# Optimization experiments

Measured on AMD Instinct MI355X. Metric: run time of the kernel, lower is better.

Reference implementation:

```python
import jax, jax.numpy as jnp
import numpy as np

D_LOW = 32
LAGS = [1, 2, 4, 8]
# Upper-triangular pair indices (offset=1), matching torch.triu_indices(d_low, d_low, 1)
IDX_I, IDX_J = np.triu_indices(D_LOW, k=1)
IDX_I = jnp.asarray(IDX_I)
IDX_J = jnp.asarray(IDX_J)
EPS = 1e-6


def setup_inputs() -> dict:
    key = jax.random.key(0)
    ks = jax.random.split(key, 7)
    b, n, d_model = 4, 4096, 1024
    d_plucker = D_LOW * (D_LOW - 1) // 2  # 496
    s = lambda fan_in: 1.0 / np.sqrt(fan_in)
    return {
        "x": jax.random.normal(ks[0], (b, n, d_model), dtype=jnp.float32),
        "W_red": jax.random.normal(ks[1], (d_model, D_LOW), dtype=jnp.float32) * s(d_model),
        "b_red": jax.random.normal(ks[2], (D_LOW,), dtype=jnp.float32) * s(d_model),
        "W_exp": jax.random.normal(ks[3], (d_plucker, d_model), dtype=jnp.float32) * s(d_plucker),
        "b_exp": jax.random.normal(ks[4], (d_model,), dtype=jnp.float32) * s(d_plucker),
        "W_gate": jax.random.normal(ks[5], (2 * d_model, d_model), dtype=jnp.float32) * s(2 * d_model),
        "b_gate": jax.random.normal(ks[6], (d_model,), dtype=jnp.float32) * s(2 * d_model),
    }


def reference(x, W_red, b_red, W_exp, b_exp, W_gate, b_gate):
    b, n, _ = x.shape
    d_plucker = D_LOW * (D_LOW - 1) // 2
    z = x @ W_red + b_red  # [b, n, d_low]
    plucker_total = jnp.zeros((b, n, d_plucker), dtype=x.dtype)
    counts = jnp.zeros((b, n, 1), dtype=x.dtype)
    for lag in LAGS:
        if lag <= 0 or lag >= n:
            continue
        z_curr = z[:, lag:, :]   # [b, n-lag, d_low]
        z_past = z[:, :-lag, :]  # [b, n-lag, d_low]
        # Antisymmetric Plucker coordinates over upper-triangular index pairs
        p = (z_curr[:, :, IDX_I] * z_past[:, :, IDX_J]
             - z_curr[:, :, IDX_J] * z_past[:, :, IDX_I])  # [b, n-lag, d_plucker]
        norm = jnp.linalg.norm(p, axis=-1, keepdims=True)
        p = p / jnp.maximum(norm, EPS)
        plucker_total = plucker_total.at[:, lag:, :].add(p)
        counts = counts.at[:, lag:, :].add(1.0)
    counts = jnp.maximum(counts, 1.0)
    plucker_avg = plucker_total / counts
    g_avg = plucker_avg @ W_exp + b_exp  # [b, n, d_model]
    concat = jnp.concatenate([x, g_avg], axis=-1)  # [b, n, 2*d_model]
    gate = jax.nn.sigmoid(concat @ W_gate + b_gate)
    return gate * x + (1.0 - gate) * g_avg
```

## Files before the change

kernel.cpp:

```cpp
#include <hip/hip_runtime.h>
#include <hip/hip_bf16.h>
#include <math.h>

#define B_DIM   4
#define N_DIM   4096
#define D_MODEL 1024
#define D_LOW   32
#define NPAIR   496
#define NROWS   (B_DIM * N_DIM)
#define KPAD3   512
#define LDA2    1536

typedef __bf16 bf16;
typedef __bf16 bf16x8 __attribute__((ext_vector_type(8)));
typedef __bf16 bf16x4 __attribute__((ext_vector_type(4)));
typedef float  f32x4  __attribute__((ext_vector_type(4)));

#define GLOAD_LDS16(g, l) __builtin_amdgcn_global_load_lds( \
    (__attribute__((address_space(1))) void*)(g),           \
    (__attribute__((address_space(3))) void*)(l), 16, 0, 0)

__global__ __launch_bounds__(256) void prep_misc(const float* __restrict__ Wr,
                                                 bf16* __restrict__ WrT,
                                                 const float* __restrict__ We,
                                                 const float* __restrict__ be,
                                                 bf16* __restrict__ WeB) {
    __shared__ float tile[32][33];
    const int bx = blockIdx.x;
    const int t  = threadIdx.x;
    if (bx < 32) {
        const int kb = bx * 32;
        {
            int k = t >> 3, c4 = (t & 7) * 4;
            float4 v = *reinterpret_cast<const float4*>(&Wr[(size_t)(kb + k) * 32 + c4]);
            tile[k][c4 + 0] = v.x; tile[k][c4 + 1] = v.y;
            tile[k][c4 + 2] = v.z; tile[k][c4 + 3] = v.w;
        }
        __syncthreads();
        {
            int c = t >> 3, kq = (t & 7) * 4;
            bf16x4 o = { (bf16)tile[kq + 0][c], (bf16)tile[kq + 1][c],
                         (bf16)tile[kq + 2][c], (bf16)tile[kq + 3][c] };
            *reinterpret_cast<bf16x4*>(&WrT[(size_t)c * 1024 + kb + kq]) = o;
        }
    } else {
        size_t o = ((size_t)(bx - 32) * 256 + t) * 4;
        int row = (int)(o >> 10), col = (int)(o & 1023);
        float4 v = {0.f, 0.f, 0.f, 0.f};
        if (row < NPAIR)       v = *reinterpret_cast<const float4*>(&We[(size_t)row * 1024 + col]);
        else if (row == NPAIR) v = *reinterpret_cast<const float4*>(&be[col]);
        bf16x4 b = { (bf16)v.x, (bf16)v.y, (bf16)v.z, (bf16)v.w };
        *reinterpret_cast<bf16x4*>(&WeB[o]) = b;
    }
}

__global__ __launch_bounds__(256) void k1_mfma(const float* __restrict__ x,
                                               const bf16* __restrict__ WrT,
                                               bf16* __restrict__ a2,
                                               float* __restrict__ zpart) {
    const int t    = threadIdx.x;
    const int wv   = t >> 6, lane = t & 63;
    const int l15  = lane & 15, lhi = lane >> 4;
    const int kc   = blockIdx.x;
    const int mt   = blockIdx.y;
    const int row  = mt * 64 + wv * 16 + l15;
    const int kb   = kc * 256;

    f32x4 accz[2] = { (f32x4){0.f,0.f,0.f,0.f}, (f32x4){0.f,0.f,0.f,0.f} };

#pragma unroll
    for (int ks = 0; ks < 8; ++ks) {
        const int k0 = kb + ks * 32 + lhi * 8;
        const float4 u0 = *reinterpret_cast<const float4*>(&x[(size_t)row * 1024 + k0]);
        const float4 u1 = *reinterpret_cast<const float4*>(&x[(size_t)row * 1024 + k0 + 4]);
        bf16x8 af = { (bf16)u0.x, (bf16)u0.y, (bf16)u0.z, (bf16)u0.w,
                      (bf16)u1.x, (bf16)u1.y, (bf16)u1.z, (bf16)u1.w };
        *reinterpret_cast<bf16x8*>(&a2[(size_t)row * LDA2 + k0]) = af;
        const bf16x8 b0 = *reinterpret_cast<const bf16x8*>(
            &WrT[(size_t)l15 * 1024 + kb + ks * 32 + lhi * 8]);
        const bf16x8 b1 = *reinterpret_cast<const bf16x8*>(
            &WrT[(size_t)(16 + l15) * 1024 + kb + ks * 32 + lhi * 8]);
        accz[0] = __builtin_amdgcn_mfma_f32_16x16x32_bf16(af, b0, accz[0], 0, 0, 0);
        accz[1] = __builtin_amdgcn_mfma_f32_16x16x32_bf16(af, b1, accz[1], 0, 0, 0);
    }
#pragma unroll
    for (int cg = 0; cg < 2; ++cg)
#pragma unroll
        for (int r = 0; r < 4; ++r) {
            const int rout = mt * 64 + wv * 16 + lhi * 4 + r;
            zpart[((size_t)kc * NROWS + rout) * 32 + cg * 16 + l15] = accz[cg][r];
        }
}

__global__ __launch_bounds__(256) void k2_plucker(const float* __restrict__ zpart,
                                                  const float* __restrict__ br,
                                                  bf16* __restrict__ a2) {
    const int wv   = threadIdx.x >> 6;
    const int lane = threadIdx.x & 63;
    const int row  = blockIdx.x * 4 + wv;
    const int t    = row & (N_DIM - 1);
    const int c    = lane & 31;
    const float bias = br[c];

    float zc = bias;
#pragma unroll
    for (int p = 0; p < 4; ++p)
        zc += zpart[((size_t)p * NROWS + row) * 32 + c];

    float zp[4];
    float red[9];
    red[0] = zc * zc;
#pragma unroll
    for (int li = 0; li < 4; ++li) {
        const int lag = 1 << li;
        float v = 0.f;
        if (t >= lag) {
            v = bias;
#pragma unroll
            for (int p = 0; p < 4; ++p)
                v += zpart[((size_t)p * NROWS + (row - lag)) * 32 + c];
        }
        zp[li] = v;
        red[1 + li] = zc * zp[li];
        red[5 + li] = zp[li] * zp[li];
    }
#pragma unroll
    for (int m = 1; m < 32; m <<= 1) {
#pragma unroll
        for (int i = 0; i < 9; ++i) red[i] += __shfl_xor(red[i], m);
    }
    float cnt = 0.f;
#pragma unroll
    for (int li = 0; li < 4; ++li) cnt += (t >= (1 << li)) ? 1.f : 0.f;
    const float inv = 1.f / fmaxf(cnt, 1.f);

    float w = 0.f;
#pragma unroll
    for (int li = 0; li < 4; ++li) {
        float n2 = fmaxf(red[0] * red[5 + li] - red[1 + li] * red[1 + li], 0.f);
        float nr = sqrtf(n2);
        float s  = (t >= (1 << li)) ? inv / fmaxf(nr, 1e-6f) : 0.f;
        w += s * zp[li];
    }

#pragma unroll
    for (int u = 0; u < 8; ++u) {
        const int k = u * 64 + lane;
        float v = 0.f;
        if (k < NPAIR) {
            int kk = k, i = 0;
            while (kk >= 31 - i) { kk -= 31 - i; ++i; }
            const int j = i + 1 + kk;
            float zci = __shfl(zc, i), zcj = __shfl(zc, j);
            float wi  = __shfl(w, i),  wj  = __shfl(w, j);
            v = zci * wj - zcj * wi;
        }
        a2[(size_t)row * LDA2 + 1024 + k] = (bf16)v;
    }
}

__global__ __launch_bounds__(256) void transpose2(const float* __restrict__ Wg,
                                                  const float* __restrict__ We,
                                                  bf16* __restrict__ BcT,
                                                  bf16* __restrict__ WgbT,
                                                  bf16* __restrict__ WeT) {
    __shared__ float tile[32][36];
    const int z = blockIdx.z;
    const float* src = (z == 0) ? Wg : (z == 1) ? (Wg + (size_t)1024 * 1024) : We;
    bf16* dst  = (z == 0) ? BcT : (z == 1) ? WgbT : WeT;
    const int Kpad = (z == 0) ? 1536 : (z == 1) ? 1024 : 512;
    const int Ksrc = (z == 2) ? NPAIR : 1024;
    const int kb = blockIdx.x * 32;
    if (kb >= Kpad) return;
    const int nb = blockIdx.y * 32;
    const int t  = threadIdx.x;
    int li = t * 4;
    int kl = li >> 5, nl = li & 31;
    float4 v = {0.f, 0.f, 0.f, 0.f};
    if (kb + kl < Ksrc)
        v = *reinterpret_cast<const float4*>(&src[(size_t)(kb + kl) * 1024 + nb + nl]);
    tile[kl][nl + 0] = v.x; tile[kl][nl + 1] = v.y;
    tile[kl][nl + 2] = v.z; tile[kl][nl + 3] = v.w;
    __syncthreads();
    int nl2 = li >> 5, kl2 = li & 31;
    bf16x4 o = { (bf16)tile[kl2 + 0][nl2], (bf16)tile[kl2 + 1][nl2],
                 (bf16)tile[kl2 + 2][nl2], (bf16)tile[kl2 + 3][nl2] };
    *reinterpret_cast<bf16x4*>(&dst[(size_t)(nb + nl2) * Kpad + kb + kl2]) = o;
}

__global__ __launch_bounds__(256) void wcomb_wave(const bf16* __restrict__ WgbT,
                                                  const bf16* __restrict__ WeB,
                                                  bf16* __restrict__ BcT) {
    const int t    = threadIdx.x;
    const int wv   = t >> 6, lane = t & 63;
    const int l15  = lane & 15, lhi = lane >> 4;
    const int kk0  = blockIdx.x * 16;
    const int n0   = blockIdx.y * 64 + wv * 16;
    f32x4 acc = (f32x4){0.f, 0.f, 0.f, 0.f};
#pragma unroll 8
    for (int kb = 0; kb < 1024; kb += 32) {
        const bf16x8 af = *reinterpret_cast<const bf16x8*>(
            &WgbT[(size_t)(n0 + l15) * 1024 + kb + lhi * 8]);
        const bf16x8 bf = *reinterpret_cast<const bf16x8*>(
            &WeB[(size_t)(kk0 + l15) * 1024 + kb + lhi * 8]);
        acc = __builtin_amdgcn_mfma_f32_16x16x32_bf16(af, bf, acc, 0, 0, 0);
    }
#pragma unroll
    for (int r = 0; r < 4; ++r) {
        const int n = n0 + lhi * 4 + r;
        BcT[(size_t)n * 1536 + 1024 + kk0 + l15] = (bf16)acc[r];
    }
}

template <int KDIM, int LDAp, int LDBp, bool GATE>
__global__ __launch_bounds__(256, 2) void gemm2c(const bf16* __restrict__ A,
                                                 const bf16* __restrict__ Bt,
                                                 const float* __restrict__ bias,
                                                 const bf16* __restrict__ gsrc,
                                                 bf16* __restrict__ gdst,
                                                 float* __restrict__ out) {
    extern __shared__ char lds[];
    const int t    = threadIdx.x;
    const int w    = t >> 6, lane = t & 63;
    const int wr   = w >> 1, wc = w & 1;
    const int l15  = lane & 15, lhi = lane >> 4;

    const int fid = blockIdx.x;
    const int xcd = fid & 7, loc = fid >> 3;
    const int mb  = (xcd * 16 + (loc >> 3)) * 128;
    const int nb  = (loc & 7) * 128;

    const int srow = t >> 3;
    const int scol = ((t & 7) ^ (srow & 7)) * 8;
    const size_t aOff = (size_t)(mb + srow) * LDAp + scol;
    const size_t bOff = (size_t)(nb + srow) * LDBp + scol;
    char* const ldsA = lds;
    char* const ldsB = lds + 32768;

#define STAGE_T(d, kb) do { \
    _Pragma("unroll") for (int q = 0; q < 4; ++q) \
        GLOAD_LDS16(A + aOff + (size_t)(q * 32) * LDAp + (kb), \
                    ldsA + (d) * 16384 + q * 4096 + t * 16); \
    _Pragma("unroll") for (int q = 0; q < 4; ++q) \
        GLOAD_LDS16(Bt + bOff + (size_t)(q * 32) * LDBp + (kb), \
                    ldsB + (d) * 16384 + q * 4096 + t * 16); } while (0)

    const int swx = (l15 & 7) << 4;

    f32x4 acc[4][4];
#pragma unroll
    for (int i = 0; i < 4; ++i)
#pragma unroll
        for (int j = 0; j < 4; ++j) acc[i][j] = (f32x4){0.f, 0.f, 0.f, 0.f};
    bf16x8 afr[4][2], bfr[4][2];

    STAGE_T(0, 0);

    const int NT = KDIM / 64;
    for (int kt = 0; kt < NT; ++kt) {
        const int d = kt & 1;
        asm volatile("s_barrier" ::: "memory");
        if (kt + 1 < NT) {
            STAGE_T(d ^ 1, (kt + 1) * 64);
            asm volatile("s_waitcnt vmcnt(8)" ::: "memory");
        } else {
            asm volatile("s_waitcnt vmcnt(0)" ::: "memory");
        }
        asm volatile("s_barrier" ::: "memory");

        const char* Ab = ldsA + d * 16384;
        const char* Bb = ldsB + d * 16384;
#pragma unroll
        for (int mf = 0; mf < 4; ++mf)
#pragma unroll
            for (int ks = 0; ks < 2; ++ks) {
                int lin = (wr * 64 + mf * 16 + l15) * 128 + ks * 64 + lhi * 16;
                afr[mf][ks] = *reinterpret_cast<const bf16x8*>(Ab + (lin ^ swx));
            }
#pragma unroll
        for (int nf = 0; nf < 4; ++nf)
#pragma unroll
            for (int ks = 0; ks < 2; ++ks) {
                int lin = (wc * 64 + nf * 16 + l15) * 128 + ks * 64 + lhi * 16;
                bfr[nf][ks] = *reinterpret_cast<const bf16x8*>(Bb + (lin ^ swx));
            }
        __builtin_amdgcn_s_setprio(1);
#pragma unroll
        for (int mf = 0; mf < 4; ++mf)
#pragma unroll
            for (int nf = 0; nf < 4; ++nf)
#pragma unroll
                for (int ks = 0; ks < 2; ++ks)
                    acc[mf][nf] = __builtin_amdgcn_mfma_f32_16x16x32_bf16(
                        afr[mf][ks], bfr[nf][ks], acc[mf][nf], 0, 0, 0);
        __builtin_amdgcn_s_setprio(0);
    }
#undef STAGE_T

#pragma unroll
    for (int mf = 0; mf < 4; ++mf) {
#pragma unroll
        for (int nf = 0; nf < 4; ++nf) {
            const int col = nb + wc * 64 + nf * 16 + l15;
            float bv = bias[col];
            if constexpr (GATE)
                bv += (float)Bt[(size_t)col * LDBp + 1024 + NPAIR];
#pragma unroll
            for (int r = 0; r < 4; ++r) {
                const int row = mb + wr * 64 + mf * 16 + lhi * 4 + r;
                float v = acc[mf][nf][r] + bv;
                if constexpr (GATE) {
                    float gate = 1.f / (1.f + expf(-v));
                    float xv = (float)A[(size_t)row * LDAp + col];
                    float gv = (float)gsrc[(size_t)row * D_MODEL + col];
                    out[(size_t)row * D_MODEL + col] = gate * xv + (1.f - gate) * gv;
                } else {
                    gdst[(size_t)row * D_MODEL + col] = (bf16)v;
                }
            }
        }
    }
}

extern "C" void kernel_launch(void* const* d_in, const int* in_sizes, int n_in,
                              void* d_out, int out_size, void* d_ws, size_t ws_size,
                              hipStream_t stream) {
    const float* x  = (const float*)d_in[0];
    const float* Wr = (const float*)d_in[1];
    const float* br = (const float*)d_in[2];
    const float* We = (const float*)d_in[3];
    const float* be = (const float*)d_in[4];
    const float* Wg = (const float*)d_in[5];
    const float* bg = (const float*)d_in[6];
    float* out = (float*)d_out;

    char* ws = (char*)d_ws;
    bf16*  gbuf  = (bf16*)(ws);
    float* zpart = (float*)(ws);
    bf16*  A2    = (bf16*)(ws + (32u << 20));
    bf16*  WeT   = (bf16*)(ws + (80u << 20));
    bf16*  BcT   = (bf16*)(ws + (81u << 20));
    bf16*  WgbT  = (bf16*)(ws + (84u << 20));
    bf16*  WeB   = (bf16*)(ws + (86u << 20));
    bf16*  WrT   = (bf16*)(ws + (88u << 20));

    (void)hipFuncSetAttribute(reinterpret_cast<const void*>(&gemm2c<KPAD3, LDA2, KPAD3, false>),
                              hipFuncAttributeMaxDynamicSharedMemorySize, 65536);
    (void)hipFuncSetAttribute(reinterpret_cast<const void*>(&gemm2c<1536, LDA2, 1536, true>),
                              hipFuncAttributeMaxDynamicSharedMemorySize, 65536);

    prep_misc<<<544, 256, 0, stream>>>(Wr, WrT, We, be, WeB);
    transpose2<<<dim3(32, 32, 3), 256, 0, stream>>>(Wg, We, BcT, WgbT, WeT);
    wcomb_wave<<<dim3(32, 16), 256, 0, stream>>>(WgbT, WeB, BcT);
    k1_mfma<<<dim3(4, 256), 256, 0, stream>>>(x, WrT, A2, zpart);
    k2_plucker<<<NROWS / 4, 256, 0, stream>>>(zpart, br, A2);

    gemm2c<KPAD3, LDA2, KPAD3, false><<<1024, 256, 65536, stream>>>(
        A2 + 1024, WeT, be, nullptr, gbuf, nullptr);
    gemm2c<1536, LDA2, 1536, true><<<1024, 256, 65536, stream>>>(
        A2, BcT, bg, gbuf, nullptr, out);
}
```

Measured before the change: 159.1 us.

## Fuse expansion GEMM into gate GEMM sharing the Plucker A-tiles

Merges the two final GEMM launches into one kernel. The kernel first runs the x part of the gate GEMM, then the Plucker K-range, where each A tile feeds both the gate weights and the expansion weights WeT into two accumulator sets. This removes the bf16 g_avg round trip through global memory and one launch, and reads the Plucker A slice once instead of twice. In exchange it doubles accumulator registers (acc2), which risks spills or lower occupancy under launch_bounds(256,2), and it uses a second swizzle layout for the 32-wide K stage.

```diff
diff --git a/kernel.cpp b/kernel.cpp
--- a/kernel.cpp
+++ b/kernel.cpp
@@ -212,12 +212,11 @@
     }
 }
 
-template <int KDIM, int LDAp, int LDBp, bool GATE>
-__global__ __launch_bounds__(256, 2) void gemm2c(const bf16* __restrict__ A,
+__global__ __launch_bounds__(256, 2) void gemmfu(const bf16* __restrict__ A,
                                                  const bf16* __restrict__ Bt,
-                                                 const float* __restrict__ bias,
-                                                 const bf16* __restrict__ gsrc,
-                                                 bf16* __restrict__ gdst,
+                                                 const bf16* __restrict__ WeT,
+                                                 const float* __restrict__ bg,
+                                                 const float* __restrict__ be,
                                                  float* __restrict__ out) {
     extern __shared__ char lds[];
     const int t    = threadIdx.x;
@@ -230,41 +229,58 @@
     const int mb  = (xcd * 16 + (loc >> 3)) * 128;
     const int nb  = (loc & 7) * 128;
 
-    const int srow = t >> 3;
-    const int scol = ((t & 7) ^ (srow & 7)) * 8;
-    const size_t aOff = (size_t)(mb + srow) * LDAp + scol;
-    const size_t bOff = (size_t)(nb + srow) * LDBp + scol;
     char* const ldsA = lds;
     char* const ldsB = lds + 32768;
 
-#define STAGE_T(d, kb) do { \
+    const int srow1 = t >> 3;
+    const int scol1 = ((t & 7) ^ (srow1 & 7)) * 8;
+    const size_t aOff1 = (size_t)(mb + srow1) * LDA2 + scol1;
+    const size_t bOff1 = (size_t)(nb + srow1) * 1536 + scol1;
+#define STAGE1(d, kb) do { \
     _Pragma("unroll") for (int q = 0; q < 4; ++q) \
-        GLOAD_LDS16(A + aOff + (size_t)(q * 32) * LDAp + (kb), \
+        GLOAD_LDS16(A + aOff1 + (size_t)(q * 32) * LDA2 + (kb), \
                     ldsA + (d) * 16384 + q * 4096 + t * 16); \
     _Pragma("unroll") for (int q = 0; q < 4; ++q) \
-        GLOAD_LDS16(Bt + bOff + (size_t)(q * 32) * LDBp + (kb), \
+        GLOAD_LDS16(Bt + bOff1 + (size_t)(q * 32) * 1536 + (kb), \
                     ldsB + (d) * 16384 + q * 4096 + t * 16); } while (0)
 
-    const int swx = (l15 & 7) << 4;
-
-    f32x4 acc[4][4];
+    const int srow2 = t >> 2;
+    const int scol2 = ((t & 3) ^ ((srow2 >> 1) & 3)) * 8;
+    const size_t aOff2 = (size_t)(mb + srow2) * LDA2 + 1024 + scol2;
+    const size_t bOff2 = (size_t)(nb + srow2) * 1536 + 1024 + scol2;
+    const size_t wOff2 = (size_t)(nb + srow2) * 512 + scol2;
+#define STAGE2(d, kb) do { \
+    GLOAD_LDS16(A + aOff2 + (kb),                        ldsA + (d) * 16384 + t * 16); \
+    GLOAD_LDS16(A + aOff2 + (size_t)64 * LDA2 + (kb),    ldsA + (d) * 16384 + 4096 + t * 16); \
+    GLOAD_LDS16(Bt + bOff2 + (kb),                       ldsB + (d) * 16384 + t * 16); \
+    GLOAD_LDS16(Bt + bOff2 + (size_t)64 * 1536 + (kb),   ldsB + (d) * 16384 + 4096 + t * 16); \
+    GLOAD_LDS16(WeT + wOff2 + (kb),                      ldsB + (d) * 16384 + 8192 + t * 16); \
+    GLOAD_LDS16(WeT + wOff2 + (size_t)64 * 512 + (kb),   ldsB + (d) * 16384 + 8192 + 4096 + t * 16); } while (0)
+
+    const int swx1 = (l15 & 7) << 4;
+    const int swr2 = ((l15 >> 1) & 3) << 4;
+
+    f32x4 acc[4][4], acc2[4][4];
 #pragma unroll
     for (int i = 0; i < 4; ++i)
 #pragma unroll
-        for (int j = 0; j < 4; ++j) acc[i][j] = (f32x4){0.f, 0.f, 0.f, 0.f};
+        for (int j = 0; j < 4; ++j) {
+            acc[i][j]  = (f32x4){0.f, 0.f, 0.f, 0.f};
+            acc2[i][j] = (f32x4){0.f, 0.f, 0.f, 0.f};
+        }
     bf16x8 afr[4][2], bfr[4][2];
 
-    STAGE_T(0, 0);
-
-    const int NT = KDIM / 64;
-    for (int kt = 0; kt < NT; ++kt) {
+    STAGE1(0, 0);
+
+    for (int kt = 0; kt < 16; ++kt) {
         const int d = kt & 1;
         asm volatile("s_barrier" ::: "memory");
-        if (kt + 1 < NT) {
-            STAGE_T(d ^ 1, (kt + 1) * 64);
+        if (kt < 15) {
+            STAGE1(d ^ 1, (kt + 1) * 64);
             asm volatile("s_waitcnt vmcnt(8)" ::: "memory");
         } else {
-            asm volatile("s_waitcnt vmcnt(0)" ::: "memory");
+            STAGE2(d ^ 1, 0);
+            asm volatile("s_waitcnt vmcnt(6)" ::: "memory");
         }
         asm volatile("s_barrier" ::: "memory");
 
@@ -275,14 +291,14 @@
 #pragma unroll
             for (int ks = 0; ks < 2; ++ks) {
                 int lin = (wr * 64 + mf * 16 + l15) * 128 + ks * 64 + lhi * 16;
-                afr[mf][ks] = *reinterpret_cast<const bf16x8*>(Ab + (lin ^ swx));
+                afr[mf][ks] = *reinterpret_cast<const bf16x8*>(Ab + (lin ^ swx1));
             }
 #pragma unroll
         for (int nf = 0; nf < 4; ++nf)
 #pragma unroll
             for (int ks = 0; ks < 2; ++ks) {
                 int lin = (wc * 64 + nf * 16 + l15) * 128 + ks * 64 + lhi * 16;
-                bfr[nf][ks] = *reinterpret_cast<const bf16x8*>(Bb + (lin ^ swx));
+                bfr[nf][ks] = *reinterpret_cast<const bf16x8*>(Bb + (lin ^ swx1));
             }
         __builtin_amdgcn_s_setprio(1);
 #pragma unroll
@@ -295,28 +311,60 @@
                         afr[mf][ks], bfr[nf][ks], acc[mf][nf], 0, 0, 0);
         __builtin_amdgcn_s_setprio(0);
     }
-#undef STAGE_T
+
+    for (int ft = 0; ft < 16; ++ft) {
+        const int d = ft & 1;
+        asm volatile("s_barrier" ::: "memory");
+        if (ft < 15) {
+            STAGE2(d ^ 1, (ft + 1) * 32);
+            asm volatile("s_waitcnt vmcnt(6)" ::: "memory");
+        } else {
+            asm volatile("s_waitcnt vmcnt(0)" ::: "memory");
+        }
+        asm volatile("s_barrier" ::: "memory");
+
+        const char* Ab = ldsA + d * 16384;
+        const char* Bb = ldsB + d * 16384;
+        bf16x8 a2f[4], bcf[4], wef[4];
+#pragma unroll
+        for (int mf = 0; mf < 4; ++mf) {
+            int lin = (wr * 64 + mf * 16 + l15) * 64 + ((lhi * 16) ^ swr2);
+            a2f[mf] = *reinterpret_cast<const bf16x8*>(Ab + lin);
+        }
+#pragma unroll
+        for (int nf = 0; nf < 4; ++nf) {
+            int lin = (wc * 64 + nf * 16 + l15) * 64 + ((lhi * 16) ^ swr2);
+            bcf[nf] = *reinterpret_cast<const bf16x8*>(Bb + lin);
+            wef[nf] = *reinterpret_cast<const bf16x8*>(Bb + 8192 + lin);
+        }
+        __builtin_amdgcn_s_setprio(1);
+#pragma unroll
+        for (int mf = 0; mf < 4; ++mf)
+#pragma unroll
+            for (int nf = 0; nf < 4; ++nf) {
+                acc[mf][nf]  = __builtin_amdgcn_mfma_f32_16x16x32_bf16(
+                    a2f[mf], bcf[nf], acc[mf][nf], 0, 0, 0);
+                acc2[mf][nf] = __builtin_amdgcn_mfma_f32_16x16x32_bf16(
+                    a2f[mf], wef[nf], acc2[mf][nf], 0, 0, 0);
+            }
+        __builtin_amdgcn_s_setprio(0);
+    }
 
 #pragma unroll
     for (int mf = 0; mf < 4; ++mf) {
 #pragma unroll
         for (int nf = 0; nf < 4; ++nf) {
             const int col = nb + wc * 64 + nf * 16 + l15;
-            float bv = bias[col];
-            if constexpr (GATE)
-                bv += (float)Bt[(size_t)col * LDBp + 1024 + NPAIR];
+            const float bgate = bg[col] + (float)Bt[(size_t)col * 1536 + 1024 + NPAIR];
+            const float bexp  = be[col];
 #pragma unroll
             for (int r = 0; r < 4; ++r) {
                 const int row = mb + wr * 64 + mf * 16 + lhi * 4 + r;
-                float v = acc[mf][nf][r] + bv;
-                if constexpr (GATE) {
-                    float gate = 1.f / (1.f + expf(-v));
-                    float xv = (float)A[(size_t)row * LDAp + col];
-                    float gv = (float)gsrc[(size_t)row * D_MODEL + col];
-                    out[(size_t)row * D_MODEL + col] = gate * xv + (1.f - gate) * gv;
-                } else {
-                    gdst[(size_t)row * D_MODEL + col] = (bf16)v;
-                }
+                const float s    = acc[mf][nf][r] + bgate;
+                const float gate = 1.f / (1.f + expf(-s));
+                const float g    = acc2[mf][nf][r] + bexp;
+                const float xv   = (float)A[(size_t)row * LDA2 + col];
+                out[(size_t)row * D_MODEL + col] = gate * xv + (1.f - gate) * g;
             }
         }
     }
@@ -335,7 +383,6 @@
     float* out = (float*)d_out;
 
     char* ws = (char*)d_ws;
-    bf16*  gbuf  = (bf16*)(ws);
     float* zpart = (float*)(ws);
     bf16*  A2    = (bf16*)(ws + (32u << 20));
     bf16*  WeT   = (bf16*)(ws + (80u << 20));
@@ -344,9 +391,7 @@
     bf16*  WeB   = (bf16*)(ws + (86u << 20));
     bf16*  WrT   = (bf16*)(ws + (88u << 20));
 
-    (void)hipFuncSetAttribute(reinterpret_cast<const void*>(&gemm2c<KPAD3, LDA2, KPAD3, false>),
-                              hipFuncAttributeMaxDynamicSharedMemorySize, 65536);
-    (void)hipFuncSetAttribute(reinterpret_cast<const void*>(&gemm2c<1536, LDA2, 1536, true>),
+    (void)hipFuncSetAttribute(reinterpret_cast<const void*>(&gemmfu),
                               hipFuncAttributeMaxDynamicSharedMemorySize, 65536);
 
     prep_misc<<<544, 256, 0, stream>>>(Wr, WrT, We, be, WeB);
@@ -355,8 +400,5 @@
     k1_mfma<<<dim3(4, 256), 256, 0, stream>>>(x, WrT, A2, zpart);
     k2_plucker<<<NROWS / 4, 256, 0, stream>>>(zpart, br, A2);
 
-    gemm2c<KPAD3, LDA2, KPAD3, false><<<1024, 256, 65536, stream>>>(
-        A2 + 1024, WeT, be, nullptr, gbuf, nullptr);
-    gemm2c<1536, LDA2, 1536, true><<<1024, 256, 65536, stream>>>(
-        A2, BcT, bg, gbuf, nullptr, out);
-}
+    gemmfu<<<1024, 256, 65536, stream>>>(A2, BcT, WeT, bg, be, out);
+}
```

Measured after the change: 153.1 us. -3.8%, faster.
